# Kernel optimization log

Measured on AMD Instinct MI355X. Metric: run time of the kernel, lower is better.

The kernel has to match this reference:

```python
import jax, jax.numpy as jnp
import numpy as np

UNITS = 1024      # LSTM hidden size
FEAT = 128        # num_features (Dense output == cell input for feedback)
T = 48            # warmup sequence length
B = 2048          # batch
OUT_STEPS = 24
S0, S1 = 0, 128   # output_indices[0] : output_indices[-1]+1


def setup_inputs() -> dict:
    key = jax.random.key(0)
    k0, k1, k2, k3 = jax.random.split(key, 4)
    inputs = jax.random.normal(k0, (B, T, FEAT), dtype=jnp.float32)
    # Keras LSTMCell params: kernel [F,4U], recurrent_kernel [U,4U], bias [4U] (gate order i,f,c,o)
    kernel = jax.random.normal(k1, (FEAT, 4 * UNITS), dtype=jnp.float32) * 0.05
    recurrent_kernel = jax.random.normal(k2, (UNITS, 4 * UNITS), dtype=jnp.float32) * 0.02
    bias = jnp.zeros((4 * UNITS,), dtype=jnp.float32)
    dense_w = jax.random.normal(k3, (UNITS, FEAT), dtype=jnp.float32) * 0.03
    dense_b = jnp.zeros((FEAT,), dtype=jnp.float32)
    return {"inputs": inputs, "kernel": kernel, "recurrent_kernel": recurrent_kernel,
            "bias": bias, "dense_w": dense_w, "dense_b": dense_b}


def _lstm_step(h, c, x, kernel, recurrent_kernel, bias):
    # Keras LSTMCell: z = x@W + h@U + b, gates split as (i, f, g, o)
    z = x @ kernel + h @ recurrent_kernel + bias
    i, f, g, o = jnp.split(z, 4, axis=-1)
    i = jax.nn.sigmoid(i)
    f = jax.nn.sigmoid(f)
    g = jnp.tanh(g)
    o = jax.nn.sigmoid(o)
    c_new = f * c + i * g
    h_new = o * jnp.tanh(c_new)
    return h_new, c_new


def reference(inputs, kernel, recurrent_kernel, bias, dense_w, dense_b):
    bsz = inputs.shape[0]
    h0 = jnp.zeros((bsz, UNITS), dtype=inputs.dtype)
    c0 = jnp.zeros((bsz, UNITS), dtype=inputs.dtype)

    # warmup: RNN over the input sequence, keep final state
    def warm_step(carry, x_t):
        h, c = carry
        h, c = _lstm_step(h, c, x_t, kernel, recurrent_kernel, bias)
        return (h, c), None

    (h, c), _ = jax.lax.scan(warm_step, (h0, c0), jnp.swapaxes(inputs, 0, 1))  # xs: [T,B,F]
    y = h @ dense_w + dense_b  # first prediction, [B, F]

    def dec_step(carry, _):
        h, c, y_prev = carry
        h, c = _lstm_step(h, c, y_prev, kernel, recurrent_kernel, bias)
        y_new = h @ dense_w + dense_b
        return (h, c, y_new), y_new[:, S0:S1]

    _, ys_rest = jax.lax.scan(dec_step, (h, c, y), None, length=OUT_STEPS - 1)  # [OUT-1,B,S]
    ys = jnp.concatenate([y[None, :, S0:S1], ys_rest], axis=0)  # [OUT,B,S]
    return jnp.transpose(ys, (1, 0, 2))  # [B, OUT, S]
```

## Files before the change

kernel.cpp:

```cpp
#include <hip/hip_runtime.h>
#include <math.h>

#define UNITS 1024
#define FEAT 128
#define TSEQ 48
#define BATCH 2048
#define OUT_STEPS 24
#define KTOT 1152
#define N4 4096

typedef unsigned short ushort;
typedef __attribute__((ext_vector_type(8))) short bf16x8;
typedef __attribute__((ext_vector_type(4))) float f32x4;

__device__ __forceinline__ ushort f2bf(float f) {
  unsigned u = __float_as_uint(f);
  unsigned r = (u + 0x7FFF + ((u >> 16) & 1)) >> 16;
  return (ushort)r;
}
__device__ __forceinline__ float sigm(float x) { return 1.0f / (1.0f + __expf(-x)); }
__device__ __forceinline__ float tanh_f(float x) { return 1.0f - 2.0f / (1.0f + __expf(2.0f * x)); }

__device__ __forceinline__ void gload_lds16(const void* g, void* l) {
  __builtin_amdgcn_global_load_lds(
      (const __attribute__((address_space(1))) unsigned int*)g,
      (__attribute__((address_space(3))) unsigned int*)l, 16, 0, 0);
}


__global__ __launch_bounds__(256)
void convert_inputs_kernel(const float* __restrict__ in, ushort* __restrict__ Xb) {
  const int o4 = (blockIdx.x * 256 + threadIdx.x) * 4;
  const int t = o4 >> 18;
  const int b = (o4 >> 7) & 2047;
  const int f = o4 & 127;
  const float4 v = *reinterpret_cast<const float4*>(&in[(size_t)(b * TSEQ + t) * FEAT + f]);
  union { ushort u[4]; unsigned long long ll; } w;
  w.u[0] = f2bf(v.x); w.u[1] = f2bf(v.y); w.u[2] = f2bf(v.z); w.u[3] = f2bf(v.w);
  *reinterpret_cast<unsigned long long*>(&Xb[o4]) = w.ll;
}

__global__ __launch_bounds__(256)
void prep_wF_kernel(const float* __restrict__ kW, const float* __restrict__ rW,
                    ushort* __restrict__ WpF) {
  const int g = blockIdx.x * 256 + threadIdx.x;
  const int lane = g & 63;
  const int kc = (g >> 6) % 36;
  const int cf = g / 2304;
  const int np = cf * 16 + (lane & 15);
  const int kbase = kc * 32 + (lane >> 4) * 8;
  const int u16 = np & 15, gg = (np >> 4) & 3, ugrp = np >> 6;
  const int nsrc = gg * 1024 + ugrp * 16 + u16;
  ushort v[8];
#pragma unroll
  for (int e = 0; e < 8; ++e) {
    const int k = kbase + e;
    const float f = (k < FEAT) ? kW[(size_t)k * N4 + nsrc] : rW[(size_t)(k - FEAT) * N4 + nsrc];
    v[e] = f2bf(f);
  }
  *reinterpret_cast<bf16x8*>(&WpF[(size_t)g * 8]) = *reinterpret_cast<bf16x8*>(v);
}

__global__ __launch_bounds__(256)
void prep_wd_kernel(const float* __restrict__ dw, ushort* __restrict__ Wdt) {
  const int o = blockIdx.x * 256 + threadIdx.x;
  const int n = o >> 10, k = o & 1023;
  Wdt[o] = f2bf(dw[(size_t)k * FEAT + n]);
}

__global__ __launch_bounds__(256)
void prep_b2_kernel(const float* __restrict__ bias, const float* __restrict__ db,
                    const float* __restrict__ W, float* __restrict__ b2) {
  const int n = blockIdx.x * 256 + threadIdx.x;
  float s = bias[n];
#pragma unroll 8
  for (int f = 0; f < FEAT; ++f) s += db[f] * W[(size_t)f * N4 + n];
  b2[n] = s;
}

__global__ __launch_bounds__(256)
void prep_u_kernel(const float* __restrict__ dw,
                   const float* __restrict__ W,
                   const float* __restrict__ rW,
                   ushort* __restrict__ Wp2F) {
  __shared__ float sWd[64][132];
  __shared__ float sW[128][68];
  const int tid = threadIdx.x;
  const int ugrp = blockIdx.x;
  const int k0 = blockIdx.y * 64;
  const int n0 = ugrp * 64;

#pragma unroll
  for (int p = 0; p < 8; ++p) {
    const int li = p * 256 + tid;
    const int kk = li >> 5, f4 = (li & 31) * 4;
    *reinterpret_cast<float4*>(&sWd[kk][f4]) =
        *reinterpret_cast<const float4*>(&dw[(size_t)(k0 + kk) * FEAT + f4]);
  }
#pragma unroll
  for (int p = 0; p < 32; ++p) {
    const int li = p * 256 + tid;
    const int f = li >> 6, nn = li & 63;
    const int u16 = nn & 15, gg = (nn >> 4) & 3;
    const int nsrc = gg * 1024 + ugrp * 16 + u16;
    sW[f][nn] = W[(size_t)f * N4 + nsrc];
  }
  __syncthreads();

  const int tx = tid & 15;
  const int ty = tid >> 4;
  float acc[4][4] = {};
  for (int f = 0; f < 128; ++f) {
    float a[4], b[4];
#pragma unroll
    for (int j = 0; j < 4; ++j) a[j] = sWd[tx * 4 + j][f];
#pragma unroll
    for (int i = 0; i < 4; ++i) b[i] = sW[f][ty * 4 + i];
#pragma unroll
    for (int i = 0; i < 4; ++i)
#pragma unroll
      for (int j = 0; j < 4; ++j) acc[i][j] += a[j] * b[i];
  }

#pragma unroll
  for (int i = 0; i < 4; ++i) {
    const int np = n0 + ty * 4 + i;
    const int u16 = np & 15, gg = (np >> 4) & 3;
    const int nsrc = gg * 1024 + ugrp * 16 + u16;
    const int cf = np >> 4;
#pragma unroll
    for (int j = 0; j < 4; ++j) {
      const int k = k0 + tx * 4 + j;
      const float v = rW[(size_t)k * N4 + nsrc] + acc[i][j];
      const int kc = k >> 5, lane = ((k >> 3) & 3) * 16 + (np & 15), e = k & 7;
      Wp2F[(((size_t)cf * 32 + kc) * 64 + lane) * 8 + e] = f2bf(v);
    }
  }
}

template<int KT, int NKS, bool HASX, bool ZC>
__global__ __launch_bounds__(256, 2)
void lstm_step_kernel(const ushort* __restrict__ Xc,
                      const ushort* __restrict__ Hin,
                      const ushort* __restrict__ WpF,
                      const float* __restrict__ bias,
                      float* __restrict__ CF,
                      ushort* __restrict__ Hout) {
  __shared__ alignas(16) ushort sA[2 * 8192];

  const int bid = blockIdx.x;
  const int wg = (bid & 7) * 64 + (bid >> 3);
  const int bx = wg & 15, by = wg >> 4;
  const int bm = bx * 128;
  const int bnf = by * 8;

  const int tid = threadIdx.x;
  const int wid = tid >> 6;
  const int l = tid & 63;
  const int wr = wid >> 1;
  const int wc = wid & 1;

  const int rloc = l >> 2;
  const int slot = l & 3;
  const int gsw = slot ^ ((rloc >> 1) & 3);
  const int l15 = l & 15;
  const int kg = l >> 4;
  const int nfbase = bnf + wc * 4;

  constexpr int NT = KT / 64;

  f32x4 acc[4][4] = {};
  bf16x8 bv0[2][4], bv1[2][4];

  const int R = bx * 2 + wr;
  const int U = by * 2 + wc;
  const size_t cfbase = (((size_t)R * 64 + U) * 64 + l) * 16;
  f32x4 cpre[4];
  if (!ZC) {
#pragma unroll
    for (int m = 0; m < 4; ++m)
      cpre[m] = *reinterpret_cast<const f32x4*>(CF + cfbase + m * 4);
  }

  auto STAGE_A = [&](int t) {
    const int bufofs = (t & 1) * 8192;
    const int k0base = t * 64;
#pragma unroll
    for (int q = 0; q < 4; ++q) {
      const int c = wid * 4 + q;
      const int r = (c & 7) * 16 + rloc;
      const int k0s = k0base + (c >> 3) * 32;
      const ushort* src;
      if (HASX && k0s < FEAT) src = Xc + (size_t)(bm + r) * FEAT + k0s + gsw * 8;
      else                    src = Hin + (size_t)(bm + r) * UNITS + (k0s - (HASX ? FEAT : 0)) + gsw * 8;
      gload_lds16(src, &sA[bufofs + c * 512]);
    }
  };

  auto LOADB = [&](int t, bf16x8 (&bv)[2][4]) {
#pragma unroll
    for (int kk = 0; kk < 2; ++kk)
#pragma unroll
      for (int n = 0; n < 4; ++n) {
        const size_t kc = (size_t)(t * 2 + kk);
        bv[kk][n] = *reinterpret_cast<const bf16x8*>(
            WpF + (((size_t)(nfbase + n) * NKS + kc) * 64 + l) * 8);
      }
  };

  auto COMPUTE = [&](int t, bf16x8 (&bv)[2][4]) {
    const int bufofs = (t & 1) * 8192;
    bf16x8 av[2][4];
#pragma unroll
    for (int kk = 0; kk < 2; ++kk)
#pragma unroll
      for (int m = 0; m < 4; ++m) {
        const int r = wr * 64 + m * 16 + l15;
        const int sph = kg ^ ((r >> 1) & 3);
        av[kk][m] = *reinterpret_cast<const bf16x8*>(&sA[bufofs + kk * 4096 + r * 32 + sph * 8]);
      }
    __builtin_amdgcn_s_setprio(1);
#pragma unroll
    for (int kk = 0; kk < 2; ++kk)
#pragma unroll
      for (int m = 0; m < 4; ++m)
#pragma unroll
        for (int n = 0; n < 4; ++n)
          acc[m][n] = __builtin_amdgcn_mfma_f32_16x16x32_bf16(av[kk][m], bv[kk][n], acc[m][n], 0, 0, 0);
    __builtin_amdgcn_s_setprio(0);
  };

  auto ITER = [&](int t, bf16x8 (&bvU)[2][4], bf16x8 (&bvL)[2][4], bool last) {
    if (!last) {
      STAGE_A(t + 1);
      LOADB(t + 1, bvL);
    }
    __builtin_amdgcn_sched_barrier(0);
    if (!last) asm volatile("s_waitcnt vmcnt(12)" ::: "memory");
    else       asm volatile("s_waitcnt vmcnt(0)" ::: "memory");
    asm volatile("s_barrier" ::: "memory");
    COMPUTE(t, bvU);
    asm volatile("s_barrier" ::: "memory");
  };

  STAGE_A(0);
  LOADB(0, bv0);

  for (int tp = 0; tp < (NT - 2) / 2; ++tp) {
    ITER(2 * tp, bv0, bv1, false);
    ITER(2 * tp + 1, bv1, bv0, false);
  }
  ITER(NT - 2, bv0, bv1, false);
  ITER(NT - 1, bv1, bv0, true);

  const int unit = U * 16 + l15;
  const float bi = bias[unit];
  const float bf_ = bias[1024 + unit];
  const float bg = bias[2048 + unit];
  const float bo = bias[3072 + unit];

#pragma unroll
  for (int m = 0; m < 4; ++m) {
    const int rowb = bm + wr * 64 + m * 16 + kg * 4;
    f32x4 cout;
#pragma unroll
    for (int j = 0; j < 4; ++j) {
      const float i_ = sigm(acc[m][0][j] + bi);
      const float f_ = sigm(acc[m][1][j] + bf_);
      const float g_ = tanh_f(acc[m][2][j] + bg);
      const float o_ = sigm(acc[m][3][j] + bo);
      const float cn = ZC ? (i_ * g_) : (f_ * cpre[m][j] + i_ * g_);
      cout[j] = cn;
      Hout[(size_t)(rowb + j) * UNITS + unit] = f2bf(o_ * tanh_f(cn));
    }
    *reinterpret_cast<f32x4*>(CF + cfbase + m * 4) = cout;
  }
}

__global__ __launch_bounds__(256)
void dense_all_kernel(const ushort* __restrict__ Hall,
                      const ushort* __restrict__ Wdt,
                      const float* __restrict__ db,
                      float* __restrict__ out) {
  __shared__ alignas(16) ushort sA[2][64 * 32];
  __shared__ alignas(16) ushort sB[2][128 * 32];

  const int bm = blockIdx.x * 64;
  const int tid = threadIdx.x;
  const int wid = tid >> 6;
  const int l = tid & 63;
  const int wr = wid >> 1;
  const int wc = wid & 1;

  const int rloc = l >> 2;
  const int slot = l & 3;
  const int gsw = slot ^ ((rloc >> 1) & 3);
  const int l15 = l & 15;
  const int kg = l >> 4;

  f32x4 acc[2][4] = {};

  auto STAGE = [&](int k0s, int bsel) {
#pragma unroll
    for (int q = 0; q < 3; ++q) {
      const int c = wid * 3 + q;
      if (c < 4) {
        const int r = c * 16 + rloc;
        gload_lds16(Hall + (size_t)(bm + r) * UNITS + k0s + gsw * 8, &sA[bsel][c * 512]);
      } else {
        const int cb = c - 4;
        const int r = cb * 16 + rloc;
        gload_lds16(Wdt + (size_t)r * UNITS + k0s + gsw * 8, &sB[bsel][cb * 512]);
      }
    }
  };

  STAGE(0, 0);
  __syncthreads();
  int cur = 0;
  for (int t = 0; t < 32; ++t) {
    if (t + 1 < 32) STAGE((t + 1) * 32, cur ^ 1);

    bf16x8 av[2], bv[4];
#pragma unroll
    for (int m = 0; m < 2; ++m) {
      const int r = wr * 32 + m * 16 + l15;
      const int sph = kg ^ ((r >> 1) & 3);
      av[m] = *reinterpret_cast<const bf16x8*>(&sA[cur][r * 32 + sph * 8]);
    }
#pragma unroll
    for (int n = 0; n < 4; ++n) {
      const int r = wc * 64 + n * 16 + l15;
      const int sph = kg ^ ((r >> 1) & 3);
      bv[n] = *reinterpret_cast<const bf16x8*>(&sB[cur][r * 32 + sph * 8]);
    }
#pragma unroll
    for (int m = 0; m < 2; ++m)
#pragma unroll
      for (int n = 0; n < 4; ++n)
        acc[m][n] = __builtin_amdgcn_mfma_f32_16x16x32_bf16(av[m], bv[n], acc[m][n], 0, 0, 0);

    __syncthreads();
    cur ^= 1;
  }

#pragma unroll
  for (int n = 0; n < 4; ++n) {
    const int f = wc * 64 + n * 16 + l15;
    const float bb = db[f];
#pragma unroll
    for (int m = 0; m < 2; ++m) {
#pragma unroll
      for (int j = 0; j < 4; ++j) {
        const int r = bm + wr * 32 + m * 16 + kg * 4 + j;
        const int s = r >> 11, b = r & 2047;
        out[((size_t)b * OUT_STEPS + s) * FEAT + f] = acc[m][n][j] + bb;
      }
    }
  }
}

extern "C" void kernel_launch(void* const* d_in, const int* in_sizes, int n_in,
                              void* d_out, int out_size, void* d_ws, size_t ws_size,
                              hipStream_t stream) {
  const float* inputs  = (const float*)d_in[0];
  const float* kernelW = (const float*)d_in[1];
  const float* recW    = (const float*)d_in[2];
  const float* bias    = (const float*)d_in[3];
  const float* dw      = (const float*)d_in[4];
  const float* db      = (const float*)d_in[5];
  float* out = (float*)d_out;

  char* ws = (char*)d_ws;
  float*  CF   = (float*)ws;
  ushort* Xb   = (ushort*)(ws + 8388608);
  ushort* Wp2F = Xb;
  ushort* Hb0  = (ushort*)(ws + 33554432);
  ushort* Hb1  = (ushort*)(ws + 37748736);
  ushort* WpF  = (ushort*)(ws + 41943040);
  ushort* Wdt  = (ushort*)(ws + 51380224);
  float*  b2   = (float*)(ws + 51642368);
  ushort* Hall = (ushort*)(ws + 51658752);
  ushort* Hb[2] = {Hb0, Hb1};
  const size_t HSLOT = (size_t)BATCH * UNITS;

  convert_inputs_kernel<<<TSEQ * BATCH * FEAT / 1024, 256, 0, stream>>>(inputs, Xb);
  prep_wF_kernel<<<(N4 / 16) * 36 * 64 / 256, 256, 0, stream>>>(kernelW, recW, WpF);
  prep_wd_kernel<<<FEAT * UNITS / 256, 256, 0, stream>>>(dw, Wdt);
  prep_b2_kernel<<<N4 / 256, 256, 0, stream>>>(bias, db, kernelW, b2);

  lstm_step_kernel<128, 36, true, true><<<512, 256, 0, stream>>>(
      Xb, Hb0 , WpF, bias, CF, Hb1);
  int cur = 1;
  for (int t = 1; t < TSEQ; ++t) {
    ushort* hout = (t == TSEQ - 1) ? Hall : Hb[cur ^ 1];
    lstm_step_kernel<KTOT, 36, true, false><<<512, 256, 0, stream>>>(
        Xb + (size_t)t * BATCH * FEAT, Hb[cur], WpF, bias, CF, hout);
    cur ^= 1;
  }
  prep_u_kernel<<<dim3(64, 16), 256, 0, stream>>>(dw, kernelW, recW, Wp2F);

  for (int s = 1; s < OUT_STEPS; ++s) {
    lstm_step_kernel<UNITS, 32, false, false><<<512, 256, 0, stream>>>(
        nullptr, Hall + (size_t)(s - 1) * HSLOT, Wp2F, b2, CF, Hall + (size_t)s * HSLOT);
  }
  dense_all_kernel<<<(OUT_STEPS * BATCH) / 64, 256, 0, stream>>>(Hall, Wdt, db, out);
}
```

Before: 2.003 ms.

## Deepen LSTM step GEMM pipeline to triple-buffered prefetch two tiles ahead

Changes the K-loop of the LSTM step kernel from double to triple buffering. A tiles in LDS and B fragments in registers are now prefetched two iterations ahead, with vmcnt waits adjusted to keep more loads in flight. The aim is to hide more global/LDS load latency behind MFMA work. In exchange, LDS use rises from 32KB to 48KB per block and an extra register set for B fragments is held, which may reduce occupancy under launch_bounds(256,2).

```diff
diff --git a/kernel.cpp b/kernel.cpp
--- a/kernel.cpp
+++ b/kernel.cpp
@@ -146,7 +146,7 @@
                       const float* __restrict__ bias,
                       float* __restrict__ CF,
                       ushort* __restrict__ Hout) {
-  __shared__ alignas(16) ushort sA[2 * 8192];
+  __shared__ alignas(16) ushort sA[3 * 8192];
 
   const int bid = blockIdx.x;
   const int wg = (bid & 7) * 64 + (bid >> 3);
@@ -168,13 +168,16 @@
   const int nfbase = bnf + wc * 4;
 
   constexpr int NT = KT / 64;
+  constexpr int S = NT - 2;
+  constexpr int G = S / 3;
+  constexpr int R = S % 3;
 
   f32x4 acc[4][4] = {};
-  bf16x8 bv0[2][4], bv1[2][4];
-
-  const int R = bx * 2 + wr;
+  bf16x8 bv0[2][4], bv1[2][4], bv2[2][4];
+
+  const int Rr = bx * 2 + wr;
   const int U = by * 2 + wc;
-  const size_t cfbase = (((size_t)R * 64 + U) * 64 + l) * 16;
+  const size_t cfbase = (((size_t)Rr * 64 + U) * 64 + l) * 16;
   f32x4 cpre[4];
   if (!ZC) {
 #pragma unroll
@@ -182,8 +185,8 @@
       cpre[m] = *reinterpret_cast<const f32x4*>(CF + cfbase + m * 4);
   }
 
-  auto STAGE_A = [&](int t) {
-    const int bufofs = (t & 1) * 8192;
+  auto STAGE_A = [&](int t, int buf) {
+    const int bufofs = buf * 8192;
     const int k0base = t * 64;
 #pragma unroll
     for (int q = 0; q < 4; ++q) {
@@ -208,50 +211,64 @@
       }
   };
 
-  auto COMPUTE = [&](int t, bf16x8 (&bv)[2][4]) {
-    const int bufofs = (t & 1) * 8192;
-    bf16x8 av[2][4];
-#pragma unroll
-    for (int kk = 0; kk < 2; ++kk)
+  auto COMPUTE = [&](bf16x8 (&bv)[2][4], int buf) {
+    const int bufofs = buf * 8192;
+    __builtin_amdgcn_s_setprio(1);
+#pragma unroll
+    for (int kk = 0; kk < 2; ++kk) {
+      bf16x8 av[4];
 #pragma unroll
       for (int m = 0; m < 4; ++m) {
         const int r = wr * 64 + m * 16 + l15;
         const int sph = kg ^ ((r >> 1) & 3);
-        av[kk][m] = *reinterpret_cast<const bf16x8*>(&sA[bufofs + kk * 4096 + r * 32 + sph * 8]);
+        av[m] = *reinterpret_cast<const bf16x8*>(&sA[bufofs + kk * 4096 + r * 32 + sph * 8]);
       }
-    __builtin_amdgcn_s_setprio(1);
-#pragma unroll
-    for (int kk = 0; kk < 2; ++kk)
 #pragma unroll
       for (int m = 0; m < 4; ++m)
 #pragma unroll
         for (int n = 0; n < 4; ++n)
-          acc[m][n] = __builtin_amdgcn_mfma_f32_16x16x32_bf16(av[kk][m], bv[kk][n], acc[m][n], 0, 0, 0);
+          acc[m][n] = __builtin_amdgcn_mfma_f32_16x16x32_bf16(av[m], bv[kk][n], acc[m][n], 0, 0, 0);
+    }
     __builtin_amdgcn_s_setprio(0);
   };
 
-  auto ITER = [&](int t, bf16x8 (&bvU)[2][4], bf16x8 (&bvL)[2][4], bool last) {
-    if (!last) {
-      STAGE_A(t + 1);
-      LOADB(t + 1, bvL);
+  auto ITER = [&](int t, bf16x8 (&bvC)[2][4], bf16x8 (&bvL)[2][4],
+                  int cb, int lb, int mode) {
+    if (mode == 0) {
+      STAGE_A(t + 2, lb);
+      LOADB(t + 2, bvL);
     }
     __builtin_amdgcn_sched_barrier(0);
-    if (!last) asm volatile("s_waitcnt vmcnt(12)" ::: "memory");
-    else       asm volatile("s_waitcnt vmcnt(0)" ::: "memory");
+    if (mode == 0)      asm volatile("s_waitcnt vmcnt(24)" ::: "memory");
+    else if (mode == 1) asm volatile("s_waitcnt vmcnt(12)" ::: "memory");
+    else                asm volatile("s_waitcnt vmcnt(0)" ::: "memory");
     asm volatile("s_barrier" ::: "memory");
-    COMPUTE(t, bvU);
+    COMPUTE(bvC, cb);
     asm volatile("s_barrier" ::: "memory");
   };
 
-  STAGE_A(0);
-  LOADB(0, bv0);
-
-  for (int tp = 0; tp < (NT - 2) / 2; ++tp) {
-    ITER(2 * tp, bv0, bv1, false);
-    ITER(2 * tp + 1, bv1, bv0, false);
-  }
-  ITER(NT - 2, bv0, bv1, false);
-  ITER(NT - 1, bv1, bv0, true);
+  STAGE_A(0, 0); LOADB(0, bv0);
+  STAGE_A(1, 1); LOADB(1, bv1);
+
+  int t = 0;
+  for (int g = 0; g < G; ++g) {
+    ITER(t, bv0, bv2, 0, 2, 0); ++t;
+    ITER(t, bv1, bv0, 1, 0, 0); ++t;
+    ITER(t, bv2, bv1, 2, 1, 0); ++t;
+  }
+  if constexpr (R == 0) {
+    ITER(t, bv0, bv0, 0, 0, 1); ++t;
+    ITER(t, bv1, bv1, 1, 1, 2); ++t;
+  } else if constexpr (R == 1) {
+    ITER(t, bv0, bv2, 0, 2, 0); ++t;
+    ITER(t, bv1, bv1, 1, 1, 1); ++t;
+    ITER(t, bv2, bv2, 2, 2, 2); ++t;
+  } else {
+    ITER(t, bv0, bv2, 0, 2, 0); ++t;
+    ITER(t, bv1, bv0, 1, 0, 0); ++t;
+    ITER(t, bv2, bv2, 2, 2, 1); ++t;
+    ITER(t, bv0, bv0, 0, 0, 2); ++t;
+  }
 
   const int unit = U * 16 + l15;
   const float bi = bias[unit];
```

New measurement: 2.141 ms. +6.8%, slower.

## Store activations in MFMA fragment layout and drop LDS staging

Applied to the files above, without the earlier changes.

The input and hidden-state buffers, and the dense weight, are now stored pre-swizzled in the MFMA fragment order. Each wave can therefore load its A and B operands straight from global memory as 16-byte vectors. The LDS double-buffer pipeline, its barriers and the async global-to-LDS loads are removed from both the LSTM step and the dense kernel. The LSTM epilogue writes h scattered into the fragment layout, and the dense kernel now uses a 128-row tile. The intent is to cut LDS traffic and synchronisation. In exchange, operand loads depend on cache hits with no explicit prefetch, and the h stores become scattered 2-byte writes.

```diff
diff --git a/kernel.cpp b/kernel.cpp
--- a/kernel.cpp
+++ b/kernel.cpp
@@ -6,7 +6,6 @@
 #define TSEQ 48
 #define BATCH 2048
 #define OUT_STEPS 24
-#define KTOT 1152
 #define N4 4096
 
 typedef unsigned short ushort;
@@ -21,23 +20,24 @@
 __device__ __forceinline__ float sigm(float x) { return 1.0f / (1.0f + __expf(-x)); }
 __device__ __forceinline__ float tanh_f(float x) { return 1.0f - 2.0f / (1.0f + __expf(2.0f * x)); }
 
-__device__ __forceinline__ void gload_lds16(const void* g, void* l) {
-  __builtin_amdgcn_global_load_lds(
-      (const __attribute__((address_space(1))) unsigned int*)g,
-      (__attribute__((address_space(3))) unsigned int*)l, 16, 0, 0);
-}
-
-
-__global__ __launch_bounds__(256)
-void convert_inputs_kernel(const float* __restrict__ in, ushort* __restrict__ Xb) {
-  const int o4 = (blockIdx.x * 256 + threadIdx.x) * 4;
-  const int t = o4 >> 18;
-  const int b = (o4 >> 7) & 2047;
-  const int f = o4 & 127;
-  const float4 v = *reinterpret_cast<const float4*>(&in[(size_t)(b * TSEQ + t) * FEAT + f]);
-  union { ushort u[4]; unsigned long long ll; } w;
-  w.u[0] = f2bf(v.x); w.u[1] = f2bf(v.y); w.u[2] = f2bf(v.z); w.u[3] = f2bf(v.w);
-  *reinterpret_cast<unsigned long long*>(&Xb[o4]) = w.ll;
+
+
+__global__ __launch_bounds__(256)
+void convert_inputs_kernel(const float* __restrict__ in, ushort* __restrict__ XF) {
+  const int g = blockIdx.x * 256 + threadIdx.x;
+  const int lane = g & 63;
+  const int kc = (g >> 6) & 3;
+  const int rf = (g >> 8) & 127;
+  const int t = g >> 15;
+  const int b = rf * 16 + (lane & 15);
+  const int f = kc * 32 + ((lane >> 4) & 3) * 8;
+  const float* src = &in[((size_t)b * TSEQ + t) * FEAT + f];
+  const float4 v0 = *reinterpret_cast<const float4*>(src);
+  const float4 v1 = *reinterpret_cast<const float4*>(src + 4);
+  ushort v[8];
+  v[0] = f2bf(v0.x); v[1] = f2bf(v0.y); v[2] = f2bf(v0.z); v[3] = f2bf(v0.w);
+  v[4] = f2bf(v1.x); v[5] = f2bf(v1.y); v[6] = f2bf(v1.z); v[7] = f2bf(v1.w);
+  *reinterpret_cast<bf16x8*>(&XF[(size_t)g * 8]) = *reinterpret_cast<bf16x8*>(v);
 }
 
 __global__ __launch_bounds__(256)
@@ -48,7 +48,7 @@
   const int kc = (g >> 6) % 36;
   const int cf = g / 2304;
   const int np = cf * 16 + (lane & 15);
-  const int kbase = kc * 32 + (lane >> 4) * 8;
+  const int kbase = kc * 32 + ((lane >> 4) & 3) * 8;
   const int u16 = np & 15, gg = (np >> 4) & 3, ugrp = np >> 6;
   const int nsrc = gg * 1024 + ugrp * 16 + u16;
   ushort v[8];
@@ -62,10 +62,17 @@
 }
 
 __global__ __launch_bounds__(256)
-void prep_wd_kernel(const float* __restrict__ dw, ushort* __restrict__ Wdt) {
-  const int o = blockIdx.x * 256 + threadIdx.x;
-  const int n = o >> 10, k = o & 1023;
-  Wdt[o] = f2bf(dw[(size_t)k * FEAT + n]);
+void prep_wdF_kernel(const float* __restrict__ dw, ushort* __restrict__ WdtF) {
+  const int g = blockIdx.x * 256 + threadIdx.x;
+  const int lane = g & 63;
+  const int kc = (g >> 6) & 31;
+  const int cf = g >> 11;
+  const int col = cf * 16 + (lane & 15);
+  const int kb = kc * 32 + ((lane >> 4) & 3) * 8;
+  ushort v[8];
+#pragma unroll
+  for (int e = 0; e < 8; ++e) v[e] = f2bf(dw[(size_t)(kb + e) * FEAT + col]);
+  *reinterpret_cast<bf16x8*>(&WdtF[(size_t)g * 8]) = *reinterpret_cast<bf16x8*>(v);
 }
 
 __global__ __launch_bounds__(256)
@@ -138,130 +145,90 @@
   }
 }
 
-template<int KT, int NKS, bool HASX, bool ZC>
+template<int KCH, int NKS, bool HASX, bool ZC>
 __global__ __launch_bounds__(256, 2)
-void lstm_step_kernel(const ushort* __restrict__ Xc,
-                      const ushort* __restrict__ Hin,
-                      const ushort* __restrict__ WpF,
+void lstm_step_kernel(const ushort* __restrict__ XF,
+                      const ushort* __restrict__ HF,
+                      const ushort* __restrict__ WF,
                       const float* __restrict__ bias,
                       float* __restrict__ CF,
-                      ushort* __restrict__ Hout) {
-  __shared__ alignas(16) ushort sA[2 * 8192];
-
+                      ushort* __restrict__ HoutF) {
   const int bid = blockIdx.x;
   const int wg = (bid & 7) * 64 + (bid >> 3);
   const int bx = wg & 15, by = wg >> 4;
-  const int bm = bx * 128;
-  const int bnf = by * 8;
 
   const int tid = threadIdx.x;
   const int wid = tid >> 6;
   const int l = tid & 63;
-  const int wr = wid >> 1;
-  const int wc = wid & 1;
-
-  const int rloc = l >> 2;
-  const int slot = l & 3;
-  const int gsw = slot ^ ((rloc >> 1) & 3);
-  const int l15 = l & 15;
-  const int kg = l >> 4;
-  const int nfbase = bnf + wc * 4;
-
-  constexpr int NT = KT / 64;
+  const int wr = wid >> 1, wc = wid & 1;
+  const int l15 = l & 15, kg = l >> 4;
+
+  const int rfb = bx * 8 + wr * 4;
+  const int cfb = by * 8 + wc * 4;
 
   f32x4 acc[4][4] = {};
-  bf16x8 bv0[2][4], bv1[2][4];
-
-  const int R = bx * 2 + wr;
+
+  if (HASX) {
+#pragma unroll
+    for (int kc = 0; kc < 4; ++kc) {
+      bf16x8 av[4], bv[4];
+#pragma unroll
+      for (int m = 0; m < 4; ++m)
+        av[m] = *reinterpret_cast<const bf16x8*>(
+            XF + (((size_t)(rfb + m) * 4 + kc) * 64 + l) * 8);
+#pragma unroll
+      for (int n = 0; n < 4; ++n)
+        bv[n] = *reinterpret_cast<const bf16x8*>(
+            WF + (((size_t)(cfb + n) * NKS + kc) * 64 + l) * 8);
+#pragma unroll
+      for (int m = 0; m < 4; ++m)
+#pragma unroll
+        for (int n = 0; n < 4; ++n)
+          acc[m][n] = __builtin_amdgcn_mfma_f32_16x16x32_bf16(av[m], bv[n], acc[m][n], 0, 0, 0);
+    }
+  }
+
+#pragma unroll 4
+  for (int kc = 0; kc < KCH; ++kc) {
+    bf16x8 av[4], bv[4];
+#pragma unroll
+    for (int m = 0; m < 4; ++m)
+      av[m] = *reinterpret_cast<const bf16x8*>(
+          HF + (((size_t)(rfb + m) * 32 + kc) * 64 + l) * 8);
+#pragma unroll
+    for (int n = 0; n < 4; ++n)
+      bv[n] = *reinterpret_cast<const bf16x8*>(
+          WF + (((size_t)(cfb + n) * NKS + (HASX ? 4 : 0) + kc) * 64 + l) * 8);
+#pragma unroll
+    for (int m = 0; m < 4; ++m)
+#pragma unroll
+      for (int n = 0; n < 4; ++n)
+        acc[m][n] = __builtin_amdgcn_mfma_f32_16x16x32_bf16(av[m], bv[n], acc[m][n], 0, 0, 0);
+  }
+
   const int U = by * 2 + wc;
-  const size_t cfbase = (((size_t)R * 64 + U) * 64 + l) * 16;
-  f32x4 cpre[4];
-  if (!ZC) {
-#pragma unroll
-    for (int m = 0; m < 4; ++m)
-      cpre[m] = *reinterpret_cast<const f32x4*>(CF + cfbase + m * 4);
-  }
-
-  auto STAGE_A = [&](int t) {
-    const int bufofs = (t & 1) * 8192;
-    const int k0base = t * 64;
-#pragma unroll
-    for (int q = 0; q < 4; ++q) {
-      const int c = wid * 4 + q;
-      const int r = (c & 7) * 16 + rloc;
-      const int k0s = k0base + (c >> 3) * 32;
-      const ushort* src;
-      if (HASX && k0s < FEAT) src = Xc + (size_t)(bm + r) * FEAT + k0s + gsw * 8;
-      else                    src = Hin + (size_t)(bm + r) * UNITS + (k0s - (HASX ? FEAT : 0)) + gsw * 8;
-      gload_lds16(src, &sA[bufofs + c * 512]);
-    }
-  };
-
-  auto LOADB = [&](int t, bf16x8 (&bv)[2][4]) {
-#pragma unroll
-    for (int kk = 0; kk < 2; ++kk)
-#pragma unroll
-      for (int n = 0; n < 4; ++n) {
-        const size_t kc = (size_t)(t * 2 + kk);
-        bv[kk][n] = *reinterpret_cast<const bf16x8*>(
-            WpF + (((size_t)(nfbase + n) * NKS + kc) * 64 + l) * 8);
-      }
-  };
-
-  auto COMPUTE = [&](int t, bf16x8 (&bv)[2][4]) {
-    const int bufofs = (t & 1) * 8192;
-    bf16x8 av[2][4];
-#pragma unroll
-    for (int kk = 0; kk < 2; ++kk)
-#pragma unroll
-      for (int m = 0; m < 4; ++m) {
-        const int r = wr * 64 + m * 16 + l15;
-        const int sph = kg ^ ((r >> 1) & 3);
-        av[kk][m] = *reinterpret_cast<const bf16x8*>(&sA[bufofs + kk * 4096 + r * 32 + sph * 8]);
-      }
-    __builtin_amdgcn_s_setprio(1);
-#pragma unroll
-    for (int kk = 0; kk < 2; ++kk)
-#pragma unroll
-      for (int m = 0; m < 4; ++m)
-#pragma unroll
-        for (int n = 0; n < 4; ++n)
-          acc[m][n] = __builtin_amdgcn_mfma_f32_16x16x32_bf16(av[kk][m], bv[kk][n], acc[m][n], 0, 0, 0);
-    __builtin_amdgcn_s_setprio(0);
-  };
-
-  auto ITER = [&](int t, bf16x8 (&bvU)[2][4], bf16x8 (&bvL)[2][4], bool last) {
-    if (!last) {
-      STAGE_A(t + 1);
-      LOADB(t + 1, bvL);
-    }
-    __builtin_amdgcn_sched_barrier(0);
-    if (!last) asm volatile("s_waitcnt vmcnt(12)" ::: "memory");
-    else       asm volatile("s_waitcnt vmcnt(0)" ::: "memory");
-    asm volatile("s_barrier" ::: "memory");
-    COMPUTE(t, bvU);
-    asm volatile("s_barrier" ::: "memory");
-  };
-
-  STAGE_A(0);
-  LOADB(0, bv0);
-
-  for (int tp = 0; tp < (NT - 2) / 2; ++tp) {
-    ITER(2 * tp, bv0, bv1, false);
-    ITER(2 * tp + 1, bv1, bv0, false);
-  }
-  ITER(NT - 2, bv0, bv1, false);
-  ITER(NT - 1, bv1, bv0, true);
-
   const int unit = U * 16 + l15;
   const float bi = bias[unit];
   const float bf_ = bias[1024 + unit];
   const float bg = bias[2048 + unit];
   const float bo = bias[3072 + unit];
 
+  const int Rr = bx * 2 + wr;
+  const size_t cfbase = (((size_t)Rr * 64 + U) * 64 + l) * 16;
+  const int kcu = unit >> 5;
+  const int lxb = ((unit >> 3) & 3) * 16;
+  const int eu = unit & 7;
+
+  f32x4 cpre[4];
+  if (!ZC) {
+#pragma unroll
+    for (int m = 0; m < 4; ++m)
+      cpre[m] = *reinterpret_cast<const f32x4*>(CF + cfbase + m * 4);
+  }
+
 #pragma unroll
   for (int m = 0; m < 4; ++m) {
-    const int rowb = bm + wr * 64 + m * 16 + kg * 4;
+    const size_t hfrag = (((size_t)(rfb + m) * 32 + kcu) * 64);
     f32x4 cout;
 #pragma unroll
     for (int j = 0; j < 4; ++j) {
@@ -271,90 +238,57 @@
       const float o_ = sigm(acc[m][3][j] + bo);
       const float cn = ZC ? (i_ * g_) : (f_ * cpre[m][j] + i_ * g_);
       cout[j] = cn;
-      Hout[(size_t)(rowb + j) * UNITS + unit] = f2bf(o_ * tanh_f(cn));
+      HoutF[(hfrag + lxb + kg * 4 + j) * 8 + eu] = f2bf(o_ * tanh_f(cn));
     }
     *reinterpret_cast<f32x4*>(CF + cfbase + m * 4) = cout;
   }
 }
 
-__global__ __launch_bounds__(256)
-void dense_all_kernel(const ushort* __restrict__ Hall,
-                      const ushort* __restrict__ Wdt,
-                      const float* __restrict__ db,
-                      float* __restrict__ out) {
-  __shared__ alignas(16) ushort sA[2][64 * 32];
-  __shared__ alignas(16) ushort sB[2][128 * 32];
-
-  const int bm = blockIdx.x * 64;
+__global__ __launch_bounds__(256, 2)
+void dense_allF_kernel(const ushort* __restrict__ HallF,
+                       const ushort* __restrict__ WdtF,
+                       const float* __restrict__ db,
+                       float* __restrict__ out) {
+  const int bid = blockIdx.x;
   const int tid = threadIdx.x;
   const int wid = tid >> 6;
   const int l = tid & 63;
-  const int wr = wid >> 1;
-  const int wc = wid & 1;
-
-  const int rloc = l >> 2;
-  const int slot = l & 3;
-  const int gsw = slot ^ ((rloc >> 1) & 3);
-  const int l15 = l & 15;
-  const int kg = l >> 4;
-
-  f32x4 acc[2][4] = {};
-
-  auto STAGE = [&](int k0s, int bsel) {
-#pragma unroll
-    for (int q = 0; q < 3; ++q) {
-      const int c = wid * 3 + q;
-      if (c < 4) {
-        const int r = c * 16 + rloc;
-        gload_lds16(Hall + (size_t)(bm + r) * UNITS + k0s + gsw * 8, &sA[bsel][c * 512]);
-      } else {
-        const int cb = c - 4;
-        const int r = cb * 16 + rloc;
-        gload_lds16(Wdt + (size_t)r * UNITS + k0s + gsw * 8, &sB[bsel][cb * 512]);
-      }
-    }
-  };
-
-  STAGE(0, 0);
-  __syncthreads();
-  int cur = 0;
-  for (int t = 0; t < 32; ++t) {
-    if (t + 1 < 32) STAGE((t + 1) * 32, cur ^ 1);
-
-    bf16x8 av[2], bv[4];
-#pragma unroll
-    for (int m = 0; m < 2; ++m) {
-      const int r = wr * 32 + m * 16 + l15;
-      const int sph = kg ^ ((r >> 1) & 3);
-      av[m] = *reinterpret_cast<const bf16x8*>(&sA[cur][r * 32 + sph * 8]);
-    }
-#pragma unroll
-    for (int n = 0; n < 4; ++n) {
-      const int r = wc * 64 + n * 16 + l15;
-      const int sph = kg ^ ((r >> 1) & 3);
-      bv[n] = *reinterpret_cast<const bf16x8*>(&sB[cur][r * 32 + sph * 8]);
-    }
-#pragma unroll
-    for (int m = 0; m < 2; ++m)
+  const int wr = wid >> 1, wc = wid & 1;
+  const int l15 = l & 15, kg = l >> 4;
+  const int rfb = bid * 8 + wr * 4;
+  const int cfb = wc * 4;
+
+  f32x4 acc[4][4] = {};
+
+#pragma unroll 4
+  for (int kc = 0; kc < 32; ++kc) {
+    bf16x8 av[4], bv[4];
+#pragma unroll
+    for (int m = 0; m < 4; ++m)
+      av[m] = *reinterpret_cast<const bf16x8*>(
+          HallF + (((size_t)(rfb + m) * 32 + kc) * 64 + l) * 8);
+#pragma unroll
+    for (int n = 0; n < 4; ++n)
+      bv[n] = *reinterpret_cast<const bf16x8*>(
+          WdtF + (((size_t)(cfb + n) * 32 + kc) * 64 + l) * 8);
+#pragma unroll
+    for (int m = 0; m < 4; ++m)
 #pragma unroll
       for (int n = 0; n < 4; ++n)
         acc[m][n] = __builtin_amdgcn_mfma_f32_16x16x32_bf16(av[m], bv[n], acc[m][n], 0, 0, 0);
-
-    __syncthreads();
-    cur ^= 1;
   }
 
 #pragma unroll
   for (int n = 0; n < 4; ++n) {
-    const int f = wc * 64 + n * 16 + l15;
-    const float bb = db[f];
-#pragma unroll
-    for (int m = 0; m < 2; ++m) {
+    const int col = (cfb + n) * 16 + l15;
+    const float bb = db[col];
+#pragma unroll
+    for (int m = 0; m < 4; ++m) {
 #pragma unroll
       for (int j = 0; j < 4; ++j) {
-        const int r = bm + wr * 32 + m * 16 + kg * 4 + j;
-        const int s = r >> 11, b = r & 2047;
-        out[((size_t)b * OUT_STEPS + s) * FEAT + f] = acc[m][n][j] + bb;
+        const int row = bid * 128 + wr * 64 + m * 16 + kg * 4 + j;
+        const int s = row >> 11, b = row & 2047;
+        out[((size_t)b * OUT_STEPS + s) * FEAT + col] = acc[m][n][j] + bb;
       }
     }
   }
@@ -372,37 +306,38 @@
   float* out = (float*)d_out;
 
   char* ws = (char*)d_ws;
-  float*  CF   = (float*)ws;
-  ushort* Xb   = (ushort*)(ws + 8388608);
-  ushort* Wp2F = Xb;
-  ushort* Hb0  = (ushort*)(ws + 33554432);
-  ushort* Hb1  = (ushort*)(ws + 37748736);
-  ushort* WpF  = (ushort*)(ws + 41943040);
-  ushort* Wdt  = (ushort*)(ws + 51380224);
-  float*  b2   = (float*)(ws + 51642368);
-  ushort* Hall = (ushort*)(ws + 51658752);
-  ushort* Hb[2] = {Hb0, Hb1};
-  const size_t HSLOT = (size_t)BATCH * UNITS;
-
-  convert_inputs_kernel<<<TSEQ * BATCH * FEAT / 1024, 256, 0, stream>>>(inputs, Xb);
-  prep_wF_kernel<<<(N4 / 16) * 36 * 64 / 256, 256, 0, stream>>>(kernelW, recW, WpF);
-  prep_wd_kernel<<<FEAT * UNITS / 256, 256, 0, stream>>>(dw, Wdt);
+  float*  CF    = (float*)ws;
+  ushort* XF    = (ushort*)(ws + 8388608);
+  ushort* Wp2F  = XF;
+  ushort* HbF0  = (ushort*)(ws + 33554432);
+  ushort* HbF1  = (ushort*)(ws + 37748736);
+  ushort* WpF   = (ushort*)(ws + 41943040);
+  ushort* WdtF  = (ushort*)(ws + 51380224);
+  float*  b2    = (float*)(ws + 51642368);
+  ushort* HallF = (ushort*)(ws + 51658752);
+  ushort* HbF[2] = {HbF0, HbF1};
+  const size_t HSLOT = (size_t)128 * 32 * 512;
+  const size_t XSLOT = (size_t)128 * 4 * 512;
+
+  convert_inputs_kernel<<<TSEQ * 128 * 4 * 64 / 256, 256, 0, stream>>>(inputs, XF);
+  prep_wF_kernel<<<256 * 36 * 64 / 256, 256, 0, stream>>>(kernelW, recW, WpF);
+  prep_wdF_kernel<<<8 * 32 * 64 / 256, 256, 0, stream>>>(dw, WdtF);
   prep_b2_kernel<<<N4 / 256, 256, 0, stream>>>(bias, db, kernelW, b2);
 
-  lstm_step_kernel<128, 36, true, true><<<512, 256, 0, stream>>>(
-      Xb, Hb0 , WpF, bias, CF, Hb1);
+  lstm_step_kernel<0, 36, true, true><<<512, 256, 0, stream>>>(
+      XF, HbF0 , WpF, bias, CF, HbF1);
   int cur = 1;
   for (int t = 1; t < TSEQ; ++t) {
-    ushort* hout = (t == TSEQ - 1) ? Hall : Hb[cur ^ 1];
-    lstm_step_kernel<KTOT, 36, true, false><<<512, 256, 0, stream>>>(
-        Xb + (size_t)t * BATCH * FEAT, Hb[cur], WpF, bias, CF, hout);
+    ushort* hout = (t == TSEQ - 1) ? HallF : HbF[cur ^ 1];
+    lstm_step_kernel<32, 36, true, false><<<512, 256, 0, stream>>>(
+        XF + (size_t)t * XSLOT, HbF[cur], WpF, bias, CF, hout);
     cur ^= 1;
   }
   prep_u_kernel<<<dim3(64, 16), 256, 0, stream>>>(dw, kernelW, recW, Wp2F);
 
   for (int s = 1; s < OUT_STEPS; ++s) {
-    lstm_step_kernel<UNITS, 32, false, false><<<512, 256, 0, stream>>>(
-        nullptr, Hall + (size_t)(s - 1) * HSLOT, Wp2F, b2, CF, Hall + (size_t)s * HSLOT);
-  }
-  dense_all_kernel<<<(OUT_STEPS * BATCH) / 64, 256, 0, stream>>>(Hall, Wdt, db, out);
-}
+    lstm_step_kernel<32, 32, false, false><<<512, 256, 0, stream>>>(
+        nullptr, HallF + (size_t)(s - 1) * HSLOT, Wp2F, b2, CF, HallF + (size_t)s * HSLOT);
+  }
+  dense_allF_kernel<<<(OUT_STEPS * BATCH) / 128, 256, 0, stream>>>(HallF, WdtF, db, out);
+}
```

After: 2.746 ms. 37.0% more time.
